# Kernel tuning notes

Hardware: AMD Instinct MI355X
Metric: run time of the kernel (lower is better)

The kernel has to match this reference:

```python
import jax, jax.numpy as jnp
import numpy as np

HIDDEN = 64
NUM_LAYERS = 6
BN_EPS = 1e-5


def setup_inputs() -> dict:
    key = jax.random.key(0)
    N, M = 1024, 1024
    num_nodes = N + M
    ks = jax.random.split(key, 12)
    x = jax.random.normal(ks[0], (num_nodes, 2), dtype=jnp.float32)
    # complete bipartite edges: (a, N+b) for all a in [0,N), b in [0,M), row-major so view(N,M) is meaningful
    row = jnp.repeat(jnp.arange(N, dtype=jnp.int64), M)
    col = N + jnp.tile(jnp.arange(M, dtype=jnp.int64), N)
    edge_index = jnp.stack([row, col], axis=0)
    s = 1.0 / np.sqrt(HIDDEN)
    return {
        "x": x,
        "edge_index": edge_index,
        "in_w": jax.random.normal(ks[1], (2, HIDDEN), jnp.float32) * 0.5,
        "in_b": jnp.zeros((HIDDEN,), jnp.float32),
        "conv_w": jax.random.normal(ks[2], (NUM_LAYERS, HIDDEN, HIDDEN), jnp.float32) * s,
        "conv_b": jnp.zeros((NUM_LAYERS, HIDDEN), jnp.float32),
        "bn_gamma": jnp.ones((NUM_LAYERS, HIDDEN), jnp.float32),
        "bn_beta": jnp.zeros((NUM_LAYERS, HIDDEN), jnp.float32),
        "out_w": jax.random.normal(ks[3], (2 * HIDDEN, 1), jnp.float32) * s,
        "out_b": jnp.zeros((1,), jnp.float32),
        "N": N,
        "M": M,
    }


def reference(x, edge_index, in_w, in_b, conv_w, conv_b, bn_gamma, bn_beta, out_w, out_b, N, M):
    num_nodes = x.shape[0]
    # GCN normalization with added self-loops (PyG GCNConv defaults)
    loops = jnp.arange(num_nodes, dtype=edge_index.dtype)
    row = jnp.concatenate([edge_index[0], loops])
    col = jnp.concatenate([edge_index[1], loops])
    deg = jax.ops.segment_sum(jnp.ones_like(col, dtype=x.dtype), col, num_segments=num_nodes)
    dinv = jnp.where(deg > 0, jax.lax.rsqrt(deg), 0.0)
    norm = dinv[row] * dinv[col]  # [E+num_nodes]

    h = jax.nn.relu(x @ in_w + in_b)
    for i in range(NUM_LAYERS):
        h_res = h
        hw = h @ conv_w[i]
        agg = jax.ops.segment_sum(hw[row] * norm[:, None], col, num_segments=num_nodes)
        h = agg + conv_b[i]
        # BatchNorm1d in training mode: batch stats, biased variance
        mu = h.mean(axis=0)
        var = ((h - mu) ** 2).mean(axis=0)
        h = (h - mu) * jax.lax.rsqrt(var + BN_EPS) * bn_gamma[i] + bn_beta[i]
        h = jax.nn.relu(h)
        if i > 0 and i % 2 == 1:
            h = h + h_res

    ef = jnp.concatenate([h[edge_index[0]], h[edge_index[1]]], axis=1)  # [E, 2H]
    scores = (ef @ out_w + out_b)[:, 0]
    return scores.reshape(N, M)
```

## Files before the change

kernel.cpp:

```cpp
#include <hip/hip_runtime.h>


#define HIDDEN 64
#define NNODES 2048

__device__ __forceinline__ float relu_(float x) { return x > 0.f ? x : 0.f; }

__global__ __launch_bounds__(256) void k_init(const float* __restrict__ x,
                                              const float* __restrict__ in_w,
                                              const float* __restrict__ in_b,
                                              float* __restrict__ h) {
    int gid = blockIdx.x * 256 + threadIdx.x;
    int node = gid >> 3;
    int f0 = (gid & 7) * 8;
    float x0 = x[node * 2 + 0], x1 = x[node * 2 + 1];
    float vals[8];
#pragma unroll
    for (int j = 0; j < 8; j++) {
        int f = f0 + j;
        vals[j] = relu_(fmaf(x0, in_w[f], fmaf(x1, in_w[64 + f], in_b[f])));
    }
    *(float4*)(h + node * 64 + f0)     = make_float4(vals[0], vals[1], vals[2], vals[3]);
    *(float4*)(h + node * 64 + f0 + 4) = make_float4(vals[4], vals[5], vals[6], vals[7]);
}

__global__ __launch_bounds__(256) void k_conv(const float* __restrict__ h,
                                              const float* __restrict__ W,
                                              float* __restrict__ hw,
                                              float* __restrict__ S_part,
                                              float* __restrict__ Q_part) {
    __shared__ float Wl[64 * 64];
    __shared__ float hl[64 * 68];
    __shared__ float hwl[64 * 68];
    const int t = threadIdx.x, b = blockIdx.x;

#pragma unroll
    for (int j = 0; j < 4; j++) {
        int i4 = j * 256 + t;
        ((float4*)Wl)[i4] = ((const float4*)W)[i4];
    }
    {
        int nl = t >> 2;
        int c0 = (t & 3) * 16;
        const float* src = h + (b * 64 + nl) * 64 + c0;
        float* dst = hl + nl * 68 + c0;
#pragma unroll
        for (int j = 0; j < 4; j++)
            *(float4*)(dst + 4 * j) = *(const float4*)(src + 4 * j);
    }
    __syncthreads();

    const int nl = t >> 3;
    const int f0 = (t & 7) * 8;
    float acc0[8], acc1[8];
#pragma unroll
    for (int j = 0; j < 8; j++) { acc0[j] = 0.f; acc1[j] = 0.f; }

    const float* hrow0 = hl + nl * 68;
    const float* hrow1 = hl + (nl + 32) * 68;
#pragma unroll
    for (int kk = 0; kk < 64; kk += 4) {
        float4 ha = *(const float4*)(hrow0 + kk);
        float4 hb = *(const float4*)(hrow1 + kk);
        float hav[4] = {ha.x, ha.y, ha.z, ha.w};
        float hbv[4] = {hb.x, hb.y, hb.z, hb.w};
#pragma unroll
        for (int j = 0; j < 4; j++) {
            const float* wrow = Wl + (kk + j) * 64 + f0;
            float4 w0 = *(const float4*)(wrow);
            float4 w1 = *(const float4*)(wrow + 4);
            float wa[8] = {w0.x, w0.y, w0.z, w0.w, w1.x, w1.y, w1.z, w1.w};
#pragma unroll
            for (int q = 0; q < 8; q++) {
                acc0[q] = fmaf(hav[j], wa[q], acc0[q]);
                acc1[q] = fmaf(hbv[j], wa[q], acc1[q]);
            }
        }
    }

    const int n0 = b * 64 + nl, n1 = n0 + 32;
    *(float4*)(hw + n0 * 64 + f0)     = make_float4(acc0[0], acc0[1], acc0[2], acc0[3]);
    *(float4*)(hw + n0 * 64 + f0 + 4) = make_float4(acc0[4], acc0[5], acc0[6], acc0[7]);
    *(float4*)(hw + n1 * 64 + f0)     = make_float4(acc1[0], acc1[1], acc1[2], acc1[3]);
    *(float4*)(hw + n1 * 64 + f0 + 4) = make_float4(acc1[4], acc1[5], acc1[6], acc1[7]);

    *(float4*)(hwl + nl * 68 + f0)            = make_float4(acc0[0], acc0[1], acc0[2], acc0[3]);
    *(float4*)(hwl + nl * 68 + f0 + 4)        = make_float4(acc0[4], acc0[5], acc0[6], acc0[7]);
    *(float4*)(hwl + (nl + 32) * 68 + f0)     = make_float4(acc1[0], acc1[1], acc1[2], acc1[3]);
    *(float4*)(hwl + (nl + 32) * 68 + f0 + 4) = make_float4(acc1[4], acc1[5], acc1[6], acc1[7]);
    __syncthreads();

    if (t < 64) {
        float s = 0.f, q = 0.f;
#pragma unroll 8
        for (int n = 0; n < 64; n++) {
            float xv = hwl[n * 68 + t];
            s += xv;
            q = fmaf(xv, xv, q);
        }
        S_part[b * 64 + t] = s;
        Q_part[b * 64 + t] = q;
    }
}

__global__ __launch_bounds__(256) void k_bn(const float* __restrict__ hw,
                                            const float* __restrict__ cb,
                                            const float* __restrict__ gamma,
                                            const float* __restrict__ beta,
                                            const float* __restrict__ S_part,
                                            const float* __restrict__ Q_part,
                                            float* __restrict__ h,
                                            float* __restrict__ u,
                                            float* __restrict__ v,
                                            const float* __restrict__ out_w,
                                            int residual, int final_) {
    __shared__ float pA[64], sA[64], pB[64], sB[64];
    const int t = threadIdx.x;
    if (t < 64) {
        float SAv = 0.f, SBv = 0.f, QAv = 0.f, QBv = 0.f;
        for (int b2 = 0; b2 < 16; b2++)  { SAv += S_part[b2 * 64 + t]; QAv += Q_part[b2 * 64 + t]; }
        for (int b2 = 16; b2 < 32; b2++) { SBv += S_part[b2 * 64 + t]; QBv += Q_part[b2 * 64 + t]; }
        const float c1 = 9.75609756097561e-4f;
        const float c2 = 3.1234752377721214e-2f;
        float sumAgg = SAv + c1 * SBv + 1024.f * c2 * SAv;
        float sumSq  = QAv + c1 * c1 * QBv + 2.f * c1 * c2 * SAv * SBv
                     + 1024.f * c2 * c2 * SAv * SAv;
        float meanAgg = sumAgg * (1.f / 2048.f);
        float var = sumSq * (1.f / 2048.f) - meanAgg * meanAgg;
        float rstd = rsqrtf(var + 1e-5f);
        float scale = rstd * gamma[t];
        float bt = beta[t];
        (void)cb;
        pA[t] = scale;
        sA[t] = bt - meanAgg * scale;
        pB[t] = c1 * scale;
        sB[t] = bt + (c2 * SAv - meanAgg) * scale;
    }
    __syncthreads();

    const int gid = blockIdx.x * 256 + t;
    const int node = gid >> 3;
    const int f0 = (gid & 7) * 8;
    const bool isA = node < 1024;
    const float* p = isA ? pA : pB;
    const float* s = isA ? sA : sB;

    float hv[8];
    {
        float4 a = *(const float4*)(hw + node * 64 + f0);
        float4 b = *(const float4*)(hw + node * 64 + f0 + 4);
        hv[0] = a.x; hv[1] = a.y; hv[2] = a.z; hv[3] = a.w;
        hv[4] = b.x; hv[5] = b.y; hv[6] = b.z; hv[7] = b.w;
    }
    float vals[8];
#pragma unroll
    for (int j = 0; j < 8; j++)
        vals[j] = relu_(fmaf(hv[j], p[f0 + j], s[f0 + j]));

    if (residual) {
        float4 a = *(const float4*)(h + node * 64 + f0);
        float4 b = *(const float4*)(h + node * 64 + f0 + 4);
        vals[0] += a.x; vals[1] += a.y; vals[2] += a.z; vals[3] += a.w;
        vals[4] += b.x; vals[5] += b.y; vals[6] += b.z; vals[7] += b.w;
    }

    if (!final_) {
        *(float4*)(h + node * 64 + f0)     = make_float4(vals[0], vals[1], vals[2], vals[3]);
        *(float4*)(h + node * 64 + f0 + 4) = make_float4(vals[4], vals[5], vals[6], vals[7]);
    } else {
        const float* w = out_w + (isA ? 0 : 64) + f0;
        float dot = 0.f;
#pragma unroll
        for (int j = 0; j < 8; j++) dot = fmaf(vals[j], w[j], dot);
        dot += __shfl_xor(dot, 1);
        dot += __shfl_xor(dot, 2);
        dot += __shfl_xor(dot, 4);
        if ((t & 7) == 0) {
            if (isA) u[node] = dot; else v[node - 1024] = dot;
        }
    }
}

__global__ __launch_bounds__(256) void k_out(const float* __restrict__ u,
                                             const float* __restrict__ v,
                                             const float* __restrict__ out_b,
                                             float* __restrict__ out) {
    const int a = blockIdx.x;
    const int t = threadIdx.x;
    float ua = u[a] + out_b[0];
    float4 vv = ((const float4*)v)[t];
    ((float4*)(out + a * 1024))[t] =
        make_float4(ua + vv.x, ua + vv.y, ua + vv.z, ua + vv.w);
}

extern "C" void kernel_launch(void* const* d_in, const int* in_sizes, int n_in,
                              void* d_out, int out_size, void* d_ws, size_t ws_size,
                              hipStream_t stream) {
    const float* x      = (const float*)d_in[0];
    const float* in_w   = (const float*)d_in[2];
    const float* in_b   = (const float*)d_in[3];
    const float* conv_w = (const float*)d_in[4];
    const float* conv_b = (const float*)d_in[5];
    const float* bn_g   = (const float*)d_in[6];
    const float* bn_b   = (const float*)d_in[7];
    const float* out_w  = (const float*)d_in[8];
    const float* out_b  = (const float*)d_in[9];
    float* out = (float*)d_out;

    float* ws     = (float*)d_ws;
    float* h      = ws;
    float* S_part = ws + 131072;
    float* Q_part = ws + 133120;
    float* u      = ws + 135168;
    float* v      = ws + 136192;
    float* hw = out;

    k_init<<<64, 256, 0, stream>>>(x, in_w, in_b, h);
    for (int i = 0; i < 6; i++) {
        k_conv<<<32, 256, 0, stream>>>(h, conv_w + i * 4096, hw, S_part, Q_part);
        k_bn<<<64, 256, 0, stream>>>(hw, conv_b + i * 64, bn_g + i * 64, bn_b + i * 64,
                                     S_part, Q_part, h, u, v, out_w,
                                     (i & 1), (i == 5) ? 1 : 0);
    }
    k_out<<<1024, 256, 0, stream>>>(u, v, out_b, out);
}
```

Measured before the change: 130.7 us.

## Fuse all GCN layers into one persistent kernel with grid barriers

Replaces the fourteen separate launches (init, six conv and six batchnorm passes, output) with a single persistent kernel of 64 blocks. Node features stay in shared memory across layers, and software grid barriers built on atomic counters exchange the per-block BN partial sums. This removes launch overhead and the global round trips for h and hw. In exchange it adds spin-wait barriers and a memset, relies on all 64 blocks being co-resident, and reads W straight from global memory instead of staging it in LDS.

```diff
diff --git a/kernel.cpp b/kernel.cpp
--- a/kernel.cpp
+++ b/kernel.cpp
@@ -1,196 +1,170 @@
 #include <hip/hip_runtime.h>
 
 
-#define HIDDEN 64
-#define NNODES 2048
+#define NBLK 64
 
 __device__ __forceinline__ float relu_(float x) { return x > 0.f ? x : 0.f; }
 
-__global__ __launch_bounds__(256) void k_init(const float* __restrict__ x,
-                                              const float* __restrict__ in_w,
-                                              const float* __restrict__ in_b,
-                                              float* __restrict__ h) {
-    int gid = blockIdx.x * 256 + threadIdx.x;
-    int node = gid >> 3;
-    int f0 = (gid & 7) * 8;
-    float x0 = x[node * 2 + 0], x1 = x[node * 2 + 1];
-    float vals[8];
+__global__ __launch_bounds__(256, 1) void k_fused(
+    const float* __restrict__ x,
+    const float* __restrict__ in_w, const float* __restrict__ in_b,
+    const float* __restrict__ conv_w,
+    const float* __restrict__ bn_g, const float* __restrict__ bn_b,
+    const float* __restrict__ out_w, const float* __restrict__ out_b,
+    float* __restrict__ out,
+    unsigned int* __restrict__ bar,
+    float* __restrict__ part,
+    float* __restrict__ uv)
+{
+    __shared__ float hl[32 * 68];
+    __shared__ float hwl[32 * 68];
+    __shared__ float redS[4 * 64], redQ[4 * 64];
+    __shared__ float pcoef[64], scoef[64];
+
+    const int t = threadIdx.x, b = blockIdx.x;
+    const int nl = t >> 3;
+    const int fi = t & 7;
+    const int f0 = fi * 8;
+    const int node = b * 32 + nl;
+    const bool isA = b < 32;
+
+    {
+        float x0 = x[node * 2], x1 = x[node * 2 + 1];
 #pragma unroll
-    for (int j = 0; j < 8; j++) {
-        int f = f0 + j;
-        vals[j] = relu_(fmaf(x0, in_w[f], fmaf(x1, in_w[64 + f], in_b[f])));
-    }
-    *(float4*)(h + node * 64 + f0)     = make_float4(vals[0], vals[1], vals[2], vals[3]);
-    *(float4*)(h + node * 64 + f0 + 4) = make_float4(vals[4], vals[5], vals[6], vals[7]);
-}
-
-__global__ __launch_bounds__(256) void k_conv(const float* __restrict__ h,
-                                              const float* __restrict__ W,
-                                              float* __restrict__ hw,
-                                              float* __restrict__ S_part,
-                                              float* __restrict__ Q_part) {
-    __shared__ float Wl[64 * 64];
-    __shared__ float hl[64 * 68];
-    __shared__ float hwl[64 * 68];
-    const int t = threadIdx.x, b = blockIdx.x;
-
-#pragma unroll
-    for (int j = 0; j < 4; j++) {
-        int i4 = j * 256 + t;
-        ((float4*)Wl)[i4] = ((const float4*)W)[i4];
-    }
-    {
-        int nl = t >> 2;
-        int c0 = (t & 3) * 16;
-        const float* src = h + (b * 64 + nl) * 64 + c0;
-        float* dst = hl + nl * 68 + c0;
-#pragma unroll
-        for (int j = 0; j < 4; j++)
-            *(float4*)(dst + 4 * j) = *(const float4*)(src + 4 * j);
+        for (int j = 0; j < 8; j++) {
+            int f = f0 + j;
+            hl[nl * 68 + f] = relu_(fmaf(x0, in_w[f], fmaf(x1, in_w[64 + f], in_b[f])));
+        }
     }
     __syncthreads();
 
-    const int nl = t >> 3;
-    const int f0 = (t & 7) * 8;
-    float acc0[8], acc1[8];
+    for (int layer = 0; layer < 6; layer++) {
+        const float* W = conv_w + layer * 4096;
+        float acc[8];
 #pragma unroll
-    for (int j = 0; j < 8; j++) { acc0[j] = 0.f; acc1[j] = 0.f; }
+        for (int j = 0; j < 8; j++) acc[j] = 0.f;
 
-    const float* hrow0 = hl + nl * 68;
-    const float* hrow1 = hl + (nl + 32) * 68;
+#pragma unroll 4
+        for (int k = 0; k < 64; k += 4) {
+            float4 hh = *(const float4*)&hl[nl * 68 + k];
+            float hv[4] = {hh.x, hh.y, hh.z, hh.w};
 #pragma unroll
-    for (int kk = 0; kk < 64; kk += 4) {
-        float4 ha = *(const float4*)(hrow0 + kk);
-        float4 hb = *(const float4*)(hrow1 + kk);
-        float hav[4] = {ha.x, ha.y, ha.z, ha.w};
-        float hbv[4] = {hb.x, hb.y, hb.z, hb.w};
+            for (int j = 0; j < 4; j++) {
+                const float* wr = W + (k + j) * 64 + f0;
+                float4 w0 = *(const float4*)wr;
+                float4 w1 = *(const float4*)(wr + 4);
+                float wv[8] = {w0.x, w0.y, w0.z, w0.w, w1.x, w1.y, w1.z, w1.w};
 #pragma unroll
-        for (int j = 0; j < 4; j++) {
-            const float* wrow = Wl + (kk + j) * 64 + f0;
-            float4 w0 = *(const float4*)(wrow);
-            float4 w1 = *(const float4*)(wrow + 4);
-            float wa[8] = {w0.x, w0.y, w0.z, w0.w, w1.x, w1.y, w1.z, w1.w};
+                for (int q = 0; q < 8; q++) acc[q] = fmaf(hv[j], wv[q], acc[q]);
+            }
+        }
+
+        *(float4*)&hwl[nl * 68 + f0]     = make_float4(acc[0], acc[1], acc[2], acc[3]);
+        *(float4*)&hwl[nl * 68 + f0 + 4] = make_float4(acc[4], acc[5], acc[6], acc[7]);
+        __syncthreads();
+        if (t < 64) {
+            float s = 0.f, q = 0.f;
+#pragma unroll 8
+            for (int n = 0; n < 32; n++) {
+                float v = hwl[n * 68 + t];
+                s += v;
+                q = fmaf(v, v, q);
+            }
+            float* P = part + layer * 8192;
+            P[b * 64 + t] = s;
+            P[4096 + b * 64 + t] = q;
+        }
+
+        __syncthreads();
+        if (t == 0) {
+            __threadfence();
+            unsigned int* c = bar + layer * 16;
+            atomicAdd(c, 1u);
+            while (__hip_atomic_load(c, __ATOMIC_RELAXED, __HIP_MEMORY_SCOPE_AGENT) < NBLK)
+                __builtin_amdgcn_s_sleep(1);
+            __threadfence();
+        }
+        __syncthreads();
+
+        {
+            const float* P = part + layer * 8192;
+            int f = t & 63, g = t >> 6;
+            float s = 0.f, q = 0.f;
+#pragma unroll 4
+            for (int b2 = g * 16; b2 < g * 16 + 16; b2++) {
+                s += P[b2 * 64 + f];
+                q += P[4096 + b2 * 64 + f];
+            }
+            redS[g * 64 + f] = s;
+            redQ[g * 64 + f] = q;
+        }
+        __syncthreads();
+        if (t < 64) {
+            float SA = redS[t] + redS[64 + t], SB = redS[128 + t] + redS[192 + t];
+            float QA = redQ[t] + redQ[64 + t], QB = redQ[128 + t] + redQ[192 + t];
+            const float c1 = 9.75609756097561e-4f;
+            const float c2 = 3.1234752377721214e-2f;
+            float sumAgg = SA + c1 * SB + 1024.f * c2 * SA;
+            float sumSq  = QA + c1 * c1 * QB + 2.f * c1 * c2 * SA * SB
+                         + 1024.f * c2 * c2 * SA * SA;
+            float meanAgg = sumAgg * (1.f / 2048.f);
+            float var = sumSq * (1.f / 2048.f) - meanAgg * meanAgg;
+            float rstd = rsqrtf(var + 1e-5f);
+            float scale = rstd * bn_g[layer * 64 + t];
+            float bt = bn_b[layer * 64 + t];
+            if (isA) { pcoef[t] = scale;      scoef[t] = bt - meanAgg * scale; }
+            else     { pcoef[t] = c1 * scale; scoef[t] = bt + (c2 * SA - meanAgg) * scale; }
+        }
+        __syncthreads();
+
+        float vals[8];
 #pragma unroll
-            for (int q = 0; q < 8; q++) {
-                acc0[q] = fmaf(hav[j], wa[q], acc0[q]);
-                acc1[q] = fmaf(hbv[j], wa[q], acc1[q]);
-            }
+        for (int j = 0; j < 8; j++)
+            vals[j] = relu_(fmaf(acc[j], pcoef[f0 + j], scoef[f0 + j]));
+        if (layer == 1 || layer == 3 || layer == 5) {
+#pragma unroll
+            for (int j = 0; j < 8; j++) vals[j] += hl[nl * 68 + f0 + j];
+        }
+
+        if (layer < 5) {
+#pragma unroll
+            for (int j = 0; j < 8; j++) hl[nl * 68 + f0 + j] = vals[j];
+            __syncthreads();
+        } else {
+            const float* w = out_w + (isA ? 0 : 64) + f0;
+            float d = 0.f;
+#pragma unroll
+            for (int j = 0; j < 8; j++) d = fmaf(vals[j], w[j], d);
+            d += __shfl_xor(d, 1);
+            d += __shfl_xor(d, 2);
+            d += __shfl_xor(d, 4);
+            if (fi == 0) uv[node] = d;
         }
     }
 
-    const int n0 = b * 64 + nl, n1 = n0 + 32;
-    *(float4*)(hw + n0 * 64 + f0)     = make_float4(acc0[0], acc0[1], acc0[2], acc0[3]);
-    *(float4*)(hw + n0 * 64 + f0 + 4) = make_float4(acc0[4], acc0[5], acc0[6], acc0[7]);
-    *(float4*)(hw + n1 * 64 + f0)     = make_float4(acc1[0], acc1[1], acc1[2], acc1[3]);
-    *(float4*)(hw + n1 * 64 + f0 + 4) = make_float4(acc1[4], acc1[5], acc1[6], acc1[7]);
-
-    *(float4*)(hwl + nl * 68 + f0)            = make_float4(acc0[0], acc0[1], acc0[2], acc0[3]);
-    *(float4*)(hwl + nl * 68 + f0 + 4)        = make_float4(acc0[4], acc0[5], acc0[6], acc0[7]);
-    *(float4*)(hwl + (nl + 32) * 68 + f0)     = make_float4(acc1[0], acc1[1], acc1[2], acc1[3]);
-    *(float4*)(hwl + (nl + 32) * 68 + f0 + 4) = make_float4(acc1[4], acc1[5], acc1[6], acc1[7]);
     __syncthreads();
-
-    if (t < 64) {
-        float s = 0.f, q = 0.f;
-#pragma unroll 8
-        for (int n = 0; n < 64; n++) {
-            float xv = hwl[n * 68 + t];
-            s += xv;
-            q = fmaf(xv, xv, q);
-        }
-        S_part[b * 64 + t] = s;
-        Q_part[b * 64 + t] = q;
-    }
-}
-
-__global__ __launch_bounds__(256) void k_bn(const float* __restrict__ hw,
-                                            const float* __restrict__ cb,
-                                            const float* __restrict__ gamma,
-                                            const float* __restrict__ beta,
-                                            const float* __restrict__ S_part,
-                                            const float* __restrict__ Q_part,
-                                            float* __restrict__ h,
-                                            float* __restrict__ u,
-                                            float* __restrict__ v,
-                                            const float* __restrict__ out_w,
-                                            int residual, int final_) {
-    __shared__ float pA[64], sA[64], pB[64], sB[64];
-    const int t = threadIdx.x;
-    if (t < 64) {
-        float SAv = 0.f, SBv = 0.f, QAv = 0.f, QBv = 0.f;
-        for (int b2 = 0; b2 < 16; b2++)  { SAv += S_part[b2 * 64 + t]; QAv += Q_part[b2 * 64 + t]; }
-        for (int b2 = 16; b2 < 32; b2++) { SBv += S_part[b2 * 64 + t]; QBv += Q_part[b2 * 64 + t]; }
-        const float c1 = 9.75609756097561e-4f;
-        const float c2 = 3.1234752377721214e-2f;
-        float sumAgg = SAv + c1 * SBv + 1024.f * c2 * SAv;
-        float sumSq  = QAv + c1 * c1 * QBv + 2.f * c1 * c2 * SAv * SBv
-                     + 1024.f * c2 * c2 * SAv * SAv;
-        float meanAgg = sumAgg * (1.f / 2048.f);
-        float var = sumSq * (1.f / 2048.f) - meanAgg * meanAgg;
-        float rstd = rsqrtf(var + 1e-5f);
-        float scale = rstd * gamma[t];
-        float bt = beta[t];
-        (void)cb;
-        pA[t] = scale;
-        sA[t] = bt - meanAgg * scale;
-        pB[t] = c1 * scale;
-        sB[t] = bt + (c2 * SAv - meanAgg) * scale;
+    if (t == 0) {
+        __threadfence();
+        unsigned int* c = bar + 6 * 16;
+        atomicAdd(c, 1u);
+        while (__hip_atomic_load(c, __ATOMIC_RELAXED, __HIP_MEMORY_SCOPE_AGENT) < NBLK)
+            __builtin_amdgcn_s_sleep(1);
+        __threadfence();
     }
     __syncthreads();
 
-    const int gid = blockIdx.x * 256 + t;
-    const int node = gid >> 3;
-    const int f0 = (gid & 7) * 8;
-    const bool isA = node < 1024;
-    const float* p = isA ? pA : pB;
-    const float* s = isA ? sA : sB;
-
-    float hv[8];
     {
-        float4 a = *(const float4*)(hw + node * 64 + f0);
-        float4 b = *(const float4*)(hw + node * 64 + f0 + 4);
-        hv[0] = a.x; hv[1] = a.y; hv[2] = a.z; hv[3] = a.w;
-        hv[4] = b.x; hv[5] = b.y; hv[6] = b.z; hv[7] = b.w;
-    }
-    float vals[8];
+        float ob = out_b[0];
+        float4 vv = ((const float4*)(uv + 1024))[t];
+        vv.x += ob; vv.y += ob; vv.z += ob; vv.w += ob;
 #pragma unroll
-    for (int j = 0; j < 8; j++)
-        vals[j] = relu_(fmaf(hv[j], p[f0 + j], s[f0 + j]));
-
-    if (residual) {
-        float4 a = *(const float4*)(h + node * 64 + f0);
-        float4 b = *(const float4*)(h + node * 64 + f0 + 4);
-        vals[0] += a.x; vals[1] += a.y; vals[2] += a.z; vals[3] += a.w;
-        vals[4] += b.x; vals[5] += b.y; vals[6] += b.z; vals[7] += b.w;
-    }
-
-    if (!final_) {
-        *(float4*)(h + node * 64 + f0)     = make_float4(vals[0], vals[1], vals[2], vals[3]);
-        *(float4*)(h + node * 64 + f0 + 4) = make_float4(vals[4], vals[5], vals[6], vals[7]);
-    } else {
-        const float* w = out_w + (isA ? 0 : 64) + f0;
-        float dot = 0.f;
-#pragma unroll
-        for (int j = 0; j < 8; j++) dot = fmaf(vals[j], w[j], dot);
-        dot += __shfl_xor(dot, 1);
-        dot += __shfl_xor(dot, 2);
-        dot += __shfl_xor(dot, 4);
-        if ((t & 7) == 0) {
-            if (isA) u[node] = dot; else v[node - 1024] = dot;
+        for (int r = 0; r < 16; r++) {
+            int a = b * 16 + r;
+            float ua = uv[a];
+            ((float4*)(out + a * 1024))[t] =
+                make_float4(ua + vv.x, ua + vv.y, ua + vv.z, ua + vv.w);
         }
     }
-}
-
-__global__ __launch_bounds__(256) void k_out(const float* __restrict__ u,
-                                             const float* __restrict__ v,
-                                             const float* __restrict__ out_b,
-                                             float* __restrict__ out) {
-    const int a = blockIdx.x;
-    const int t = threadIdx.x;
-    float ua = u[a] + out_b[0];
-    float4 vv = ((const float4*)v)[t];
-    ((float4*)(out + a * 1024))[t] =
-        make_float4(ua + vv.x, ua + vv.y, ua + vv.z, ua + vv.w);
 }
 
 extern "C" void kernel_launch(void* const* d_in, const int* in_sizes, int n_in,
@@ -200,27 +174,17 @@
     const float* in_w   = (const float*)d_in[2];
     const float* in_b   = (const float*)d_in[3];
     const float* conv_w = (const float*)d_in[4];
-    const float* conv_b = (const float*)d_in[5];
     const float* bn_g   = (const float*)d_in[6];
     const float* bn_b   = (const float*)d_in[7];
     const float* out_w  = (const float*)d_in[8];
     const float* out_b  = (const float*)d_in[9];
     float* out = (float*)d_out;
 
-    float* ws     = (float*)d_ws;
-    float* h      = ws;
-    float* S_part = ws + 131072;
-    float* Q_part = ws + 133120;
-    float* u      = ws + 135168;
-    float* v      = ws + 136192;
-    float* hw = out;
+    unsigned int* bar = (unsigned int*)d_ws;
+    float* part = (float*)d_ws + 128;
+    float* uv   = part + 6 * 8192;
 
-    k_init<<<64, 256, 0, stream>>>(x, in_w, in_b, h);
-    for (int i = 0; i < 6; i++) {
-        k_conv<<<32, 256, 0, stream>>>(h, conv_w + i * 4096, hw, S_part, Q_part);
-        k_bn<<<64, 256, 0, stream>>>(hw, conv_b + i * 64, bn_g + i * 64, bn_b + i * 64,
-                                     S_part, Q_part, h, u, v, out_w,
-                                     (i & 1), (i == 5) ? 1 : 0);
-    }
-    k_out<<<1024, 256, 0, stream>>>(u, v, out_b, out);
+    hipMemsetAsync(d_ws, 0, 512, stream);
+    k_fused<<<NBLK, 256, 0, stream>>>(x, in_w, in_b, conv_w, bn_g, bn_b,
+                                      out_w, out_b, out, bar, part, uv);
 }
```

New measurement: 145.9 us. 11.6% more time.
